# Kernel optimization log

Hardware: AMD Instinct MI355X
Metric: run time of the kernel (lower is better)

## Reference

```python
import jax, jax.numpy as jnp
import numpy as np

H = 512          # hidden_size == input_size
K = 32768        # number of child cell inputs (lattice merge fan-in)


def setup_inputs() -> dict:
    key = jax.random.key(0)
    ks = jax.random.split(key, 8)
    s = 1.0 / np.sqrt(H)  # keep matmul outputs O(1)
    return {
        "input_": jax.random.normal(ks[0], (1, H), dtype=jnp.float32),
        "c_input": jax.random.normal(ks[1], (K, H), dtype=jnp.float32),
        "h_0": jax.random.normal(ks[2], (1, H), dtype=jnp.float32),
        "c_0": jax.random.normal(ks[3], (1, H), dtype=jnp.float32),
        "weight_ih": jax.random.normal(ks[4], (H, 3 * H), dtype=jnp.float32) * s,
        "weight_hh": jax.random.normal(ks[5], (H, 3 * H), dtype=jnp.float32) * s,
        "bias": jnp.zeros((3 * H,), dtype=jnp.float32),
        "alpha_weight_ih": jax.random.normal(ks[6], (H, H), dtype=jnp.float32) * s,
        "alpha_weight_hh": jax.random.normal(ks[7], (H, H), dtype=jnp.float32) * s,
    }


def reference(input_, c_input, h_0, c_0, weight_ih, weight_hh, bias,
              alpha_weight_ih, alpha_weight_hh):
    # Gate pre-activations: addmm(bias, h_0, W_hh) + input_ @ W_ih  -> [1, 3H]
    gates = h_0 @ weight_hh + bias + input_ @ weight_ih
    i, o, g = jnp.split(gates, 3, axis=1)        # each [1, H]
    i = jax.nn.sigmoid(i)
    o = jax.nn.sigmoid(o)
    g = jnp.tanh(g)

    # Variable-child softmax-weighted cell merge (non-empty c_input branch)
    alpha_wi = input_ @ alpha_weight_ih          # [1, H], broadcast over K
    alpha_wh = c_input @ alpha_weight_hh         # [K, H]
    alpha = jax.nn.sigmoid(alpha_wi + alpha_wh)  # [K, H]

    logits = jnp.concatenate([i, alpha], axis=0)  # [K+1, H]
    w = jnp.exp(logits)
    w = w / (w.sum(axis=0, keepdims=True) + 1e-12)

    merge = jnp.concatenate([g, c_input], axis=0)  # [K+1, H]
    c_1 = (merge * w).sum(axis=0, keepdims=True)   # [1, H]
    h_1 = o * jnp.tanh(c_1)                        # [1, H]
    return h_1, c_1
```

## Files before the change

### kernel.cpp

```cpp
#include <hip/hip_runtime.h>
#include <hip/hip_bf16.h>
#include <stdint.h>

#define Hdim 512
#define KC   32768

typedef __hip_bfloat16 bf16;
typedef __attribute__((ext_vector_type(8))) short short8;
typedef __attribute__((ext_vector_type(4))) float float4v;

__device__ __forceinline__ unsigned int pack_bf16_trunc(float e0, float e1) {
  union { float f; unsigned int u; } a, b;
  a.f = e0; b.f = e1;
  return __builtin_amdgcn_perm(b.u, a.u, 0x07060302u);
}

__global__ __launch_bounds__(256) void prep_wt_kernel(
    const float* __restrict__ input_, const float* __restrict__ h_0,
    const float* __restrict__ w_ih, const float* __restrict__ w_hh,
    const float* __restrict__ a_w_ih, const float* __restrict__ a_w_hh,
    float* __restrict__ gates, float* __restrict__ awi, bf16* __restrict__ wt) {
  __shared__ float sh[64 * 65];
  const int t = threadIdx.x;
  if (blockIdx.x < 128) {
    const int b  = blockIdx.x;
    const int jt = b & 31, dc = b >> 5;
    const int lane = t & 63, wv = t >> 6;
    float* h0s = sh;
    float* ins = sh + 128;
    float* red = sh + 256;
    if (t < 128) { h0s[t] = h_0[dc * 128 + t]; ins[t] = input_[dc * 128 + t]; }
    __syncthreads();
    float acc = 0.f;
    if (jt < 24) {
      const int j = jt * 64 + lane;
#pragma unroll 4
      for (int i = 0; i < 32; ++i) {
        const int dl = wv * 32 + i;
        const size_t d = dc * 128 + dl;
        acc += h0s[dl] * w_hh[d * 1536 + j] + ins[dl] * w_ih[d * 1536 + j];
      }
    } else {
      const int j = (jt - 24) * 64 + lane;
#pragma unroll 4
      for (int i = 0; i < 32; ++i) {
        const int dl = wv * 32 + i;
        const size_t d = dc * 128 + dl;
        acc += ins[dl] * a_w_ih[d * Hdim + j];
      }
    }
    red[wv * 64 + lane] = acc;
    __syncthreads();
    if (t < 64) {
      float s = red[t] + red[64 + t] + red[128 + t] + red[192 + t];
      if (jt < 24) atomicAdd(&gates[jt * 64 + t], s);
      else         atomicAdd(&awi[(jt - 24) * 64 + t], s);
    }
  } else {
    const int b = blockIdx.x - 128;
    const int d0 = (b & 7) * 64, h0 = (b >> 3) * 64;
    const int tx = t & 63, tw = t >> 6;
    float (*tile)[65] = (float (*)[65])sh;
#pragma unroll
    for (int r = 0; r < 16; ++r) {
      const int row = r * 4 + tw;
      tile[row][tx] = a_w_hh[(size_t)(d0 + row) * Hdim + h0 + tx];
    }
    __syncthreads();
#pragma unroll
    for (int r = 0; r < 16; ++r) {
      const int row = r * 4 + tw;
      wt[(size_t)(h0 + row) * Hdim + d0 + tx] = __float2bfloat16(tile[tx][row]);
    }
  }
}

__global__ __launch_bounds__(256) void gemm_reduce_kernel(
    const float* __restrict__ c_input, const bf16* __restrict__ WT,
    const float* __restrict__ awi,
    float* __restrict__ pw, float* __restrict__ pwc) {
  __shared__ __align__(16) bf16 As[128 * 64];
  __shared__ __align__(16) bf16 Bs[128 * 64];
  __shared__ float red_w[2][128];
  __shared__ float red_wc[2][128];

  const int tid  = threadIdx.x;
  const int lane = tid & 63;
  const int wave = tid >> 6;
  const int wm   = wave & 1;
  const int wn   = wave >> 1;
  const int lm   = lane & 15;
  const int lq   = lane >> 4;

  const int id     = blockIdx.x;
  const int kk_idx = ((id >> 5) << 3) | (id & 7);
  const int h_idx  = (id >> 3) & 3;
  const int kk0 = kk_idx * 128;
  const int h0  = h_idx * 128;

  float4v acc[4][4];
#pragma unroll
  for (int i = 0; i < 4; ++i)
#pragma unroll
    for (int j = 0; j < 4; ++j)
      acc[i][j] = (float4v){0.f, 0.f, 0.f, 0.f};

  char* AsB = (char*)As;
  char* BsB = (char*)Bs;

  for (int d0 = 0; d0 < Hdim; d0 += 64) {
#pragma unroll
    for (int j = 0; j < 8; ++j) {
      const int f = j * 256 + tid;
      const int row = f >> 4, sub = f & 15;
      float4v v = *(const float4v*)(c_input + (size_t)(kk0 + row) * Hdim + d0 + sub * 4);
      unsigned long long p = (unsigned long long)pack_bf16_trunc(v[0], v[1])
                           | ((unsigned long long)pack_bf16_trunc(v[2], v[3]) << 32);
      *(unsigned long long*)(AsB + row * 128 + (((sub >> 1) ^ (row & 7)) * 16) + (sub & 1) * 8) = p;
    }
#pragma unroll
    for (int r = 0; r < 4; ++r) {
      const int row = r * 32 + wave * 8 + (lane >> 3);
      const int g   = lane & 7;
      short8 wv8 = *(const short8*)(WT + (size_t)(h0 + row) * Hdim + d0 + g * 8);
      *(short8*)(BsB + row * 128 + ((g ^ (lane >> 3)) * 16)) = wv8;
    }
    __syncthreads();

#pragma unroll
    for (int ks = 0; ks < 2; ++ks) {
      short8 a[4], b[4];
#pragma unroll
      for (int mt = 0; mt < 4; ++mt) {
        const int row = wm * 64 + mt * 16 + lm;
        a[mt] = *(const short8*)(AsB + row * 128 + (((ks * 4 + lq) ^ (lm & 7)) * 16));
      }
#pragma unroll
      for (int nt = 0; nt < 4; ++nt) {
        const int row = wn * 64 + nt * 16 + lm;
        b[nt] = *(const short8*)(BsB + row * 128 + (((ks * 4 + lq) ^ (lm & 7)) * 16));
      }
#pragma unroll
      for (int mt = 0; mt < 4; ++mt)
#pragma unroll
        for (int nt = 0; nt < 4; ++nt)
          acc[mt][nt] = __builtin_amdgcn_mfma_f32_16x16x32_bf16(a[mt], b[nt], acc[mt][nt], 0, 0, 0);
    }
    __syncthreads();
  }

  float awi_l[4];
#pragma unroll
  for (int nt = 0; nt < 4; ++nt)
    awi_l[nt] = awi[h0 + wn * 64 + nt * 16 + lm];

  float sw[4] = {0.f, 0.f, 0.f, 0.f}, swc[4] = {0.f, 0.f, 0.f, 0.f};
#pragma unroll
  for (int nt = 0; nt < 4; ++nt) {
    const int h = h0 + wn * 64 + nt * 16 + lm;
#pragma unroll
    for (int mt = 0; mt < 4; ++mt) {
      const int kkb = kk0 + wm * 64 + mt * 16 + lq * 4;
#pragma unroll
      for (int r = 0; r < 4; ++r) {
        float v = acc[mt][nt][r] + awi_l[nt];
        float aval = 1.f / (1.f + __expf(-v));
        float e = __expf(aval);
        float c = c_input[(size_t)(kkb + r) * Hdim + h];
        sw[nt]  += e;
        swc[nt] += e * c;
      }
    }
  }
#pragma unroll
  for (int nt = 0; nt < 4; ++nt) {
    sw[nt]  += __shfl_xor(sw[nt], 16, 64);
    sw[nt]  += __shfl_xor(sw[nt], 32, 64);
    swc[nt] += __shfl_xor(swc[nt], 16, 64);
    swc[nt] += __shfl_xor(swc[nt], 32, 64);
  }
  if (lq == 0) {
#pragma unroll
    for (int nt = 0; nt < 4; ++nt) {
      red_w[wm][wn * 64 + nt * 16 + lm]  = sw[nt];
      red_wc[wm][wn * 64 + nt * 16 + lm] = swc[nt];
    }
  }
  __syncthreads();
  if (tid < 128) {
    pw[(size_t)kk_idx * Hdim + h0 + tid]  = red_w[0][tid] + red_w[1][tid];
    pwc[(size_t)kk_idx * Hdim + h0 + tid] = red_wc[0][tid] + red_wc[1][tid];
  }
}

__global__ __launch_bounds__(256) void finalize_kernel(
    const float* __restrict__ pw, const float* __restrict__ pwc,
    const float* __restrict__ gates, const float* __restrict__ bias,
    float* __restrict__ out) {
  __shared__ float rsw[4][64], rswc[4][64];
  const int t = threadIdx.x;
  const int hl = t & 63, q = t >> 6;
  const int hh = blockIdx.x * 64 + hl;
  float sw = 0.f, swc = 0.f;
#pragma unroll 4
  for (int kb = q * 64; kb < q * 64 + 64; ++kb) {
    sw  += pw[(size_t)kb * Hdim + hh];
    swc += pwc[(size_t)kb * Hdim + hh];
  }
  rsw[q][hl] = sw; rswc[q][hl] = swc;
  __syncthreads();
  if (t < 64) {
    const int h = blockIdx.x * 64 + t;
    sw  = rsw[0][t] + rsw[1][t] + rsw[2][t] + rsw[3][t];
    swc = rswc[0][t] + rswc[1][t] + rswc[2][t] + rswc[3][t];
    float ipre = gates[h] + bias[h];
    float opre = gates[Hdim + h] + bias[Hdim + h];
    float gpre = gates[2 * Hdim + h] + bias[2 * Hdim + h];
    float ei = expf(1.f / (1.f + expf(-ipre)));
    float g  = tanhf(gpre);
    float o  = 1.f / (1.f + expf(-opre));
    float denom = ei + sw + 1e-12f;
    float c1 = (ei * g + swc) / denom;
    float h1 = o * tanhf(c1);
    out[h]        = h1;
    out[Hdim + h] = c1;
  }
}

extern "C" void kernel_launch(void* const* d_in, const int* in_sizes, int n_in,
                              void* d_out, int out_size, void* d_ws, size_t ws_size,
                              hipStream_t stream) {
  const float* input_  = (const float*)d_in[0];
  const float* c_input = (const float*)d_in[1];
  const float* h_0     = (const float*)d_in[2];
  const float* w_ih    = (const float*)d_in[4];
  const float* w_hh    = (const float*)d_in[5];
  const float* bias    = (const float*)d_in[6];
  const float* a_w_ih  = (const float*)d_in[7];
  const float* a_w_hh  = (const float*)d_in[8];

  char* ws = (char*)d_ws;
  float* pw    = (float*)ws;
  float* pwc   = (float*)(ws + 512 * 1024);
  float* gates = (float*)(ws + 1024 * 1024);
  float* awi   = (float*)(ws + 1024 * 1024 + 6144);
  bf16*  WT    = (bf16*)(ws + 1024 * 1024 + 8192);

  hipMemsetAsync(ws + 1024 * 1024, 0, 8192, stream);
  hipLaunchKernelGGL(prep_wt_kernel, dim3(192), dim3(256), 0, stream,
                     input_, h_0, w_ih, w_hh, a_w_ih, a_w_hh, gates, awi, WT);
  hipLaunchKernelGGL(gemm_reduce_kernel, dim3(1024), dim3(256), 0, stream,
                     c_input, WT, awi, pw, pwc);
  hipLaunchKernelGGL(finalize_kernel, dim3(8), dim3(256), 0, stream,
                     pw, pwc, gates, bias, (float*)d_out);
}
```

Baseline: 151.1 us.

## Register-prefetch GEMM tiles, drop memset and atomics, rebalance prep and finalize

The GEMM main loop now issues the next K-slice's global loads for c_input and WT into registers before running the MFMAs on the current LDS tile. It writes them to LDS after a barrier, overlapping memory latency with compute, and adds launch_bounds occupancy hint 3. The gate prep kernel now has each block cover the full reduction dimension, so the atomics and the hipMemsetAsync are no longer needed. The finalize kernel uses 16 blocks instead of 8. The trade-offs are higher register pressure from the prefetch buffers, an extra barrier per iteration, and fewer, longer prep blocks.

```diff
diff --git a/kernel.cpp b/kernel.cpp
--- a/kernel.cpp
+++ b/kernel.cpp
@@ -13,6 +13,11 @@
   union { float f; unsigned int u; } a, b;
   a.f = e0; b.f = e1;
   return __builtin_amdgcn_perm(b.u, a.u, 0x07060302u);
+}
+
+__device__ __forceinline__ unsigned long long pack64(float4v v) {
+  return (unsigned long long)pack_bf16_trunc(v[0], v[1])
+       | ((unsigned long long)pack_bf16_trunc(v[2], v[3]) << 32);
 }
 
 __global__ __launch_bounds__(256) void prep_wt_kernel(
@@ -22,43 +27,43 @@
     float* __restrict__ gates, float* __restrict__ awi, bf16* __restrict__ wt) {
   __shared__ float sh[64 * 65];
   const int t = threadIdx.x;
-  if (blockIdx.x < 128) {
-    const int b  = blockIdx.x;
-    const int jt = b & 31, dc = b >> 5;
+  const int b = blockIdx.x;
+  if (b < 32) {
     const int lane = t & 63, wv = t >> 6;
     float* h0s = sh;
-    float* ins = sh + 128;
-    float* red = sh + 256;
-    if (t < 128) { h0s[t] = h_0[dc * 128 + t]; ins[t] = input_[dc * 128 + t]; }
+    float* ins = sh + 512;
+    float* red = sh + 1024;
+    for (int i = t; i < 512; i += 256) { h0s[i] = h_0[i]; ins[i] = input_[i]; }
     __syncthreads();
     float acc = 0.f;
-    if (jt < 24) {
-      const int j = jt * 64 + lane;
-#pragma unroll 4
-      for (int i = 0; i < 32; ++i) {
-        const int dl = wv * 32 + i;
-        const size_t d = dc * 128 + dl;
-        acc += h0s[dl] * w_hh[d * 1536 + j] + ins[dl] * w_ih[d * 1536 + j];
+    if (b < 24) {
+      const int j = b * 64 + lane;
+      const float* whh = w_hh + j;
+      const float* wih = w_ih + j;
+#pragma unroll 16
+      for (int i = 0; i < 128; ++i) {
+        const int d = wv * 128 + i;
+        acc += h0s[d] * whh[(size_t)d * 1536] + ins[d] * wih[(size_t)d * 1536];
       }
     } else {
-      const int j = (jt - 24) * 64 + lane;
-#pragma unroll 4
-      for (int i = 0; i < 32; ++i) {
-        const int dl = wv * 32 + i;
-        const size_t d = dc * 128 + dl;
-        acc += ins[dl] * a_w_ih[d * Hdim + j];
+      const int j = (b - 24) * 64 + lane;
+      const float* wai = a_w_ih + j;
+#pragma unroll 16
+      for (int i = 0; i < 128; ++i) {
+        const int d = wv * 128 + i;
+        acc += ins[d] * wai[(size_t)d * Hdim];
       }
     }
     red[wv * 64 + lane] = acc;
     __syncthreads();
     if (t < 64) {
       float s = red[t] + red[64 + t] + red[128 + t] + red[192 + t];
-      if (jt < 24) atomicAdd(&gates[jt * 64 + t], s);
-      else         atomicAdd(&awi[(jt - 24) * 64 + t], s);
+      if (b < 24) gates[b * 64 + t] = s;
+      else        awi[(b - 24) * 64 + t] = s;
     }
   } else {
-    const int b = blockIdx.x - 128;
-    const int d0 = (b & 7) * 64, h0 = (b >> 3) * 64;
+    const int bb = b - 32;
+    const int d0 = (bb & 7) * 64, h0 = (bb >> 3) * 64;
     const int tx = t & 63, tw = t >> 6;
     float (*tile)[65] = (float (*)[65])sh;
 #pragma unroll
@@ -75,7 +80,7 @@
   }
 }
 
-__global__ __launch_bounds__(256) void gemm_reduce_kernel(
+__global__ __launch_bounds__(256, 3) void gemm_reduce_kernel(
     const float* __restrict__ c_input, const bf16* __restrict__ WT,
     const float* __restrict__ awi,
     float* __restrict__ pw, float* __restrict__ pwc) {
@@ -98,6 +103,19 @@
   const int kk0 = kk_idx * 128;
   const int h0  = h_idx * 128;
 
+  char* AsB = (char*)As;
+  char* BsB = (char*)Bs;
+
+  const int sub   = tid & 15;
+  const int rbase = tid >> 4;
+  const float* aglob = c_input + (size_t)(kk0 + rbase) * Hdim + sub * 4;
+  const int a_lds = rbase * 128 + (((sub >> 1) ^ (rbase & 7)) * 16) + (sub & 1) * 8;
+
+  const int brow0 = wave * 8 + (lane >> 3);
+  const int bg    = lane & 7;
+  const bf16* bglob = WT + (size_t)(h0 + brow0) * Hdim + bg * 8;
+  const int b_lds = brow0 * 128 + ((bg ^ (lane >> 3)) * 16);
+
   float4v acc[4][4];
 #pragma unroll
   for (int i = 0; i < 4; ++i)
@@ -105,31 +123,36 @@
     for (int j = 0; j < 4; ++j)
       acc[i][j] = (float4v){0.f, 0.f, 0.f, 0.f};
 
-  char* AsB = (char*)As;
-  char* BsB = (char*)Bs;
-
-  for (int d0 = 0; d0 < Hdim; d0 += 64) {
-#pragma unroll
-    for (int j = 0; j < 8; ++j) {
-      const int f = j * 256 + tid;
-      const int row = f >> 4, sub = f & 15;
-      float4v v = *(const float4v*)(c_input + (size_t)(kk0 + row) * Hdim + d0 + sub * 4);
-      unsigned long long p = (unsigned long long)pack_bf16_trunc(v[0], v[1])
-                           | ((unsigned long long)pack_bf16_trunc(v[2], v[3]) << 32);
-      *(unsigned long long*)(AsB + row * 128 + (((sub >> 1) ^ (row & 7)) * 16) + (sub & 1) * 8) = p;
-    }
-#pragma unroll
-    for (int r = 0; r < 4; ++r) {
-      const int row = r * 32 + wave * 8 + (lane >> 3);
-      const int g   = lane & 7;
-      short8 wv8 = *(const short8*)(WT + (size_t)(h0 + row) * Hdim + d0 + g * 8);
-      *(short8*)(BsB + row * 128 + ((g ^ (lane >> 3)) * 16)) = wv8;
-    }
-    __syncthreads();
-
+  float4v ap[8];
+  short8  bp[4];
+
+#pragma unroll
+  for (int j = 0; j < 8; ++j)
+    ap[j] = *(const float4v*)(aglob + j * 16 * Hdim);
+#pragma unroll
+  for (int r = 0; r < 4; ++r)
+    bp[r] = *(const short8*)(bglob + (size_t)r * 32 * Hdim);
+#pragma unroll
+  for (int j = 0; j < 8; ++j)
+    *(unsigned long long*)(AsB + j * 2048 + a_lds) = pack64(ap[j]);
+#pragma unroll
+  for (int r = 0; r < 4; ++r)
+    *(short8*)(BsB + r * 4096 + b_lds) = bp[r];
+  __syncthreads();
+
+  for (int t = 0; t < 8; ++t) {
+    const int d0n = (t + 1) * 64;
+    if (t < 7) {
+#pragma unroll
+      for (int j = 0; j < 8; ++j)
+        ap[j] = *(const float4v*)(aglob + j * 16 * Hdim + d0n);
+#pragma unroll
+      for (int r = 0; r < 4; ++r)
+        bp[r] = *(const short8*)(bglob + (size_t)r * 32 * Hdim + d0n);
+    }
 #pragma unroll
     for (int ks = 0; ks < 2; ++ks) {
-      short8 a[4], b[4];
+      short8 a[4], bfr[4];
 #pragma unroll
       for (int mt = 0; mt < 4; ++mt) {
         const int row = wm * 64 + mt * 16 + lm;
@@ -138,13 +161,22 @@
 #pragma unroll
       for (int nt = 0; nt < 4; ++nt) {
         const int row = wn * 64 + nt * 16 + lm;
-        b[nt] = *(const short8*)(BsB + row * 128 + (((ks * 4 + lq) ^ (lm & 7)) * 16));
+        bfr[nt] = *(const short8*)(BsB + row * 128 + (((ks * 4 + lq) ^ (lm & 7)) * 16));
       }
 #pragma unroll
       for (int mt = 0; mt < 4; ++mt)
 #pragma unroll
         for (int nt = 0; nt < 4; ++nt)
-          acc[mt][nt] = __builtin_amdgcn_mfma_f32_16x16x32_bf16(a[mt], b[nt], acc[mt][nt], 0, 0, 0);
+          acc[mt][nt] = __builtin_amdgcn_mfma_f32_16x16x32_bf16(a[mt], bfr[nt], acc[mt][nt], 0, 0, 0);
+    }
+    __syncthreads();
+    if (t < 7) {
+#pragma unroll
+      for (int j = 0; j < 8; ++j)
+        *(unsigned long long*)(AsB + j * 2048 + a_lds) = pack64(ap[j]);
+#pragma unroll
+      for (int r = 0; r < 4; ++r)
+        *(short8*)(BsB + r * 4096 + b_lds) = bp[r];
     }
     __syncthreads();
   }
@@ -197,22 +229,23 @@
     const float* __restrict__ pw, const float* __restrict__ pwc,
     const float* __restrict__ gates, const float* __restrict__ bias,
     float* __restrict__ out) {
-  __shared__ float rsw[4][64], rswc[4][64];
+  __shared__ float rsw[8][32], rswc[8][32];
   const int t = threadIdx.x;
-  const int hl = t & 63, q = t >> 6;
-  const int hh = blockIdx.x * 64 + hl;
+  const int hl = t & 31, q = t >> 5;
+  const int hh = blockIdx.x * 32 + hl;
   float sw = 0.f, swc = 0.f;
-#pragma unroll 4
-  for (int kb = q * 64; kb < q * 64 + 64; ++kb) {
+#pragma unroll 8
+  for (int kb = q * 32; kb < q * 32 + 32; ++kb) {
     sw  += pw[(size_t)kb * Hdim + hh];
     swc += pwc[(size_t)kb * Hdim + hh];
   }
   rsw[q][hl] = sw; rswc[q][hl] = swc;
   __syncthreads();
-  if (t < 64) {
-    const int h = blockIdx.x * 64 + t;
-    sw  = rsw[0][t] + rsw[1][t] + rsw[2][t] + rsw[3][t];
-    swc = rswc[0][t] + rswc[1][t] + rswc[2][t] + rswc[3][t];
+  if (t < 32) {
+    const int h = blockIdx.x * 32 + t;
+    sw = 0.f; swc = 0.f;
+#pragma unroll
+    for (int q2 = 0; q2 < 8; ++q2) { sw += rsw[q2][t]; swc += rswc[q2][t]; }
     float ipre = gates[h] + bias[h];
     float opre = gates[Hdim + h] + bias[Hdim + h];
     float gpre = gates[2 * Hdim + h] + bias[2 * Hdim + h];
@@ -246,11 +279,10 @@
   float* awi   = (float*)(ws + 1024 * 1024 + 6144);
   bf16*  WT    = (bf16*)(ws + 1024 * 1024 + 8192);
 
-  hipMemsetAsync(ws + 1024 * 1024, 0, 8192, stream);
-  hipLaunchKernelGGL(prep_wt_kernel, dim3(192), dim3(256), 0, stream,
+  hipLaunchKernelGGL(prep_wt_kernel, dim3(96), dim3(256), 0, stream,
                      input_, h_0, w_ih, w_hh, a_w_ih, a_w_hh, gates, awi, WT);
   hipLaunchKernelGGL(gemm_reduce_kernel, dim3(1024), dim3(256), 0, stream,
                      c_input, WT, awi, pw, pwc);
-  hipLaunchKernelGGL(finalize_kernel, dim3(8), dim3(256), 0, stream,
+  hipLaunchKernelGGL(finalize_kernel, dim3(16), dim3(256), 0, stream,
                      pw, pwc, gates, bias, (float*)d_out);
 }
```

After: 153.3 us. About the same (+1.4%).
